# Performance work log

Hardware: AMD Instinct MI355X
Metric: run time of the kernel (lower is better)

The kernel has to match this reference:

```python
import jax, jax.numpy as jnp
import numpy as np


def setup_inputs() -> dict:
    key = jax.random.key(0)
    kq, kk, kv = jax.random.split(key, 3)
    B, L, S, H, E = 2, 2048, 2048, 8, 64
    queries = jax.random.normal(kq, (B, L, H, E), dtype=jnp.float32)
    keys = jax.random.normal(kk, (B, S, H, E), dtype=jnp.float32)
    values = jax.random.normal(kv, (B, S, H, E), dtype=jnp.float32)
    a1 = jnp.float32(1.0)
    a2 = jnp.float32(1.0)
    return {"queries": queries, "keys": keys, "values": values, "a1": a1, "a2": a2}


def reference(queries, keys, values, a1, a2):
    # queries: (B,L,H,E); keys/values: (B,S,H,E)
    E = queries.shape[-1]
    scale = 1.0 / jnp.sqrt(jnp.float32(E))
    # shared QK scores: (B,H,L,S)
    qk = jnp.einsum('blhe,bshe->bhls', queries, keys) * scale
    # sparse branch: relu^2 (dropout = identity in eval)
    ssa = jnp.square(jax.nn.relu(qk))
    ssa_out = jnp.einsum('bhls,bshd->blhd', ssa, values)
    # dense branch: softmax over keys
    dsa = jax.nn.softmax(qk, axis=-1)
    dsa_out = jnp.einsum('bhls,bshd->blhd', dsa, values)
    w1 = jnp.exp(a1)
    w2 = jnp.exp(a2)
    alpha1 = w1 / (w1 + w2)
    alpha2 = w2 / (w1 + w2)
    return alpha1 * ssa_out + alpha2 * dsa_out
```

## Files before the change

### kernel.cpp

```cpp
#include <hip/hip_runtime.h>

typedef short short4v __attribute__((ext_vector_type(4)));
typedef short short8v __attribute__((ext_vector_type(8)));
typedef float float4v __attribute__((ext_vector_type(4)));
typedef unsigned short u16;

#define NB 2
#define NL 2048
#define NS 2048
#define NH 8
#define NE 64
#define HE (NH*NE)
#define NLT (NL/64)
#define NST (NS/64)
#define TILE_U16 4096

static __device__ __forceinline__ unsigned pk2bf(float a, float b) {
  union { float f; unsigned u; } x, y; x.f = a; y.f = b;
  return __builtin_amdgcn_perm(y.u + 0x8000u, x.u + 0x8000u, 0x07060302u);
}

static __device__ __forceinline__ unsigned cvtpk(float a, float b) {
  unsigned r;
  asm("v_cvt_pk_bf16_f32 %0, %1, %2" : "=v"(r) : "v"(a), "v"(b));
  return r;
}

static __device__ __forceinline__ float fexp2(float x) {
  float r;
  asm("v_exp_f32 %0, %1" : "=v"(r) : "v"(x));
  return r;
}

#define GLD16(gp, lp) __builtin_amdgcn_global_load_lds( \
    (const __attribute__((address_space(1))) void*)(gp), \
    (__attribute__((address_space(3))) void*)(lp), 16, 0, 0)

static __device__ __forceinline__ int fK(int s) { return (s & 3) | ((s >> 1) & 4); }

__global__ __launch_bounds__(256)
void prepack(const float* __restrict__ kp, const float* __restrict__ vp,
             u16* __restrict__ kimg, u16* __restrict__ vimg)
{
  __shared__ __align__(16) u16 ldsv[TILE_U16];

  const int bid  = blockIdx.x;
  const int tile = bid >> 1;
  const int doV  = bid & 1;
  const int st = tile & (NST - 1);
  const int bh = tile >> 5;
  const int h  = bh & (NH - 1);
  const int b  = bh >> 3;
  const int s0 = st * 64;
  const size_t base = (size_t)b * NS * HE + h * NE;
  const int tid  = threadIdx.x;
  const int wv   = tid >> 6;
  const int lane = tid & 63;
  const int ln7  = lane & 7;

  if (!doV) {
    u16* kt = kimg + (size_t)tile * TILE_U16;
    for (int slot = tid; slot < 512; slot += 256) {
      const int srow = slot >> 3, p = slot & 7, c = p ^ fK(srow);
      const float* src = kp + base + (size_t)(s0 + srow) * HE + c * 8;
      float4 x0 = *(const float4*)src;
      float4 x1 = *(const float4*)(src + 4);
      unsigned d[4] = { pk2bf(x0.x, x0.y), pk2bf(x0.z, x0.w),
                        pk2bf(x1.x, x1.y), pk2bf(x1.z, x1.w) };
      *(int4*)(kt + slot * 8) = *(const int4*)d;
    }
    return;
  }

  u16* vt = vimg + (size_t)tile * TILE_U16;
  {
    const float* vcol = vp + base + (size_t)(s0 + wv * 16) * HE + lane;
    unsigned vr[8];
    #pragma unroll
    for (int jj = 0; jj < 8; ++jj)
      vr[jj] = pk2bf(vcol[(size_t)(2 * jj) * HE], vcol[(size_t)(2 * jj + 1) * HE]);
    #pragma unroll
    for (int i = 0; i < 2; ++i) {
      const int cs = (2 * wv + i) ^ ln7;
      int4 t4 = make_int4((int)vr[4*i+0], (int)vr[4*i+1],
                          (int)vr[4*i+2], (int)vr[4*i+3]);
      *(int4*)(&ldsv[lane * 64 + cs * 8]) = t4;
    }
  }
  __syncthreads();
  {
    const int4* s = (const int4*)ldsv;
    int4* dst = (int4*)vt;
    dst[tid]       = s[tid];
    dst[tid + 256] = s[tid + 256];
  }
}

__global__ __launch_bounds__(512, 4)
void assa_fwd(const float* __restrict__ qp, const u16* __restrict__ kimg,
              const u16* __restrict__ vimg, const float* __restrict__ a1p,
              const float* __restrict__ a2p, float* __restrict__ op)
{
  __shared__ __align__(16) u16 ldsb[2][2][2 * TILE_U16];

  const int tid  = threadIdx.x;
  const int wv   = tid >> 6;
  const int ws   = wv & 3;
  const int strm = wv >> 2;
  const int lane = tid & 63;
  const int ln15 = lane & 15;
  const int ln7  = lane & 7;
  const int quad = lane >> 4;

  const int bid = blockIdx.x;
  const int bh  = bid & 15;
  const int lt  = bid >> 4;
  const int h   = bh & (NH - 1);
  const int b   = bh >> 3;

  const int lbase = lt * 64 + ws * 16;

  short8v qf0, qf1;
  {
    const float qs = 0.125f * 1.44269504089f;
    const float* qrow = qp + ((size_t)(b * NL + lbase + ln15)) * HE + h * NE + quad * 8;
    float4 q0 = *(const float4*)(qrow);
    float4 q1 = *(const float4*)(qrow + 4);
    float4 q2 = *(const float4*)(qrow + 32);
    float4 q3 = *(const float4*)(qrow + 36);
    unsigned d0[4] = { pk2bf(qs*q0.x, qs*q0.y), pk2bf(qs*q0.z, qs*q0.w),
                       pk2bf(qs*q1.x, qs*q1.y), pk2bf(qs*q1.z, qs*q1.w) };
    unsigned d1[4] = { pk2bf(qs*q2.x, qs*q2.y), pk2bf(qs*q2.z, qs*q2.w),
                       pk2bf(qs*q3.x, qs*q3.y), pk2bf(qs*q3.z, qs*q3.w) };
    qf0 = *(const short8v*)d0;
    qf1 = *(const short8v*)d1;
  }

  short8v ones8;
  #pragma unroll
  for (int j = 0; j < 8; ++j) ones8[j] = (short)0x3F80;

  const size_t tbase = (size_t)bh * NST;

  float4v acc_s[4], acc_d[4], acc_l;
  #pragma unroll
  for (int t = 0; t < 4; ++t)
    #pragma unroll
    for (int r = 0; r < 4; ++r) { acc_s[t][r] = 0.0f; acc_d[t][r] = 0.0f; }
  #pragma unroll
  for (int r = 0; r < 4; ++r) acc_l[r] = 0.0f;

  auto dma_tile = [&](int st, int nb) {
    const int hf = ws & 1;
    const u16* g;
    u16* l;
    if (ws < 2) {
      g = kimg + (tbase + st) * TILE_U16 + hf * 2048 + lane * 8;
      l = &ldsb[strm][nb][hf * 2048];
    } else {
      g = vimg + (tbase + st) * TILE_U16 + hf * 2048 + lane * 8;
      l = &ldsb[strm][nb][TILE_U16 + hf * 2048];
    }
    GLD16(g,        l);
    GLD16(g +  512, l +  512);
    GLD16(g + 1024, l + 1024);
    GLD16(g + 1536, l + 1536);
  };

  dma_tile(strm, 0);

  const int rperm = 8 * (ln15 >> 2) + (ln15 & 3);
  const int fk    = (ln15 & 3) | (((ln15 >> 2) & 1) << 2);

  for (int it = 0; it < NST / 2; ++it) {
    asm volatile("s_waitcnt vmcnt(0)" ::: "memory");
    __builtin_amdgcn_s_barrier();
    asm volatile("" ::: "memory");
    if (it + 1 < NST / 2) dma_tile(2 * (it + 1) + strm, (it + 1) & 1);

    const u16* kb_l = ldsb[strm][it & 1];
    const u16* vb_l = kb_l + TILE_U16;

    #pragma unroll
    for (int U = 0; U < 2; ++U) {
      float4v sa0, sa1;
      #pragma unroll
      for (int r = 0; r < 4; ++r) { sa0[r] = 0.0f; sa1[r] = 0.0f; }
      const u16* krow0 = &kb_l[(32 * U + rperm) * 64];
      const u16* krow1 = krow0 + 4 * 64;
      short8v kf00 = *(const short8v*)(krow0 + (quad ^ fk) * 8);
      short8v kf01 = *(const short8v*)(krow0 + ((4 + quad) ^ fk) * 8);
      short8v kf10 = *(const short8v*)(krow1 + (quad ^ fk) * 8);
      short8v kf11 = *(const short8v*)(krow1 + ((4 + quad) ^ fk) * 8);
      __builtin_amdgcn_s_setprio(1);
      sa0 = __builtin_amdgcn_mfma_f32_16x16x32_bf16(kf00, qf0, sa0, 0, 0, 0);
      sa0 = __builtin_amdgcn_mfma_f32_16x16x32_bf16(kf01, qf1, sa0, 0, 0, 0);
      sa1 = __builtin_amdgcn_mfma_f32_16x16x32_bf16(kf10, qf0, sa1, 0, 0, 0);
      sa1 = __builtin_amdgcn_mfma_f32_16x16x32_bf16(kf11, qf1, sa1, 0, 0, 0);
      __builtin_amdgcn_s_setprio(0);

      float ps[8], pd[8];
      #pragma unroll
      for (int r = 0; r < 4; ++r) {
        float s0 = sa0[r], s1 = sa1[r];
        float r0 = s0 > 0.0f ? s0 : 0.0f;
        float r1 = s1 > 0.0f ? s1 : 0.0f;
        ps[r] = r0 * r0;  ps[4 + r] = r1 * r1;
        pd[r] = fexp2(s0); pd[4 + r] = fexp2(s1);
      }
      unsigned da[4] = { cvtpk(ps[0], ps[1]), cvtpk(ps[2], ps[3]),
                         cvtpk(ps[4], ps[5]), cvtpk(ps[6], ps[7]) };
      unsigned db[4] = { cvtpk(pd[0], pd[1]), cvtpk(pd[2], pd[3]),
                         cvtpk(pd[4], pd[5]), cvtpk(pd[6], pd[7]) };
      short8v as8 = *(const short8v*)da;
      short8v ad8 = *(const short8v*)db;

      __builtin_amdgcn_s_setprio(1);
      acc_l = __builtin_amdgcn_mfma_f32_16x16x32_bf16(ad8, ones8, acc_l, 0, 0, 0);

      #pragma unroll
      for (int t = 0; t < 4; ++t) {
        short8v vf = *(const short8v*)(&vb_l[(t * 16 + ln15) * 64 +
                        (((4 * U + quad) ^ ln7) * 8)]);
        acc_s[t] = __builtin_amdgcn_mfma_f32_16x16x32_bf16(as8, vf, acc_s[t], 0, 0, 0);
        acc_d[t] = __builtin_amdgcn_mfma_f32_16x16x32_bf16(ad8, vf, acc_d[t], 0, 0, 0);
      }
      __builtin_amdgcn_s_setprio(0);
    }
  }

  __syncthreads();
  float* red = (float*)&ldsb[0][0][0];
  const int idx = ws * 64 + lane;
  if (strm == 1) {
    #pragma unroll
    for (int t = 0; t < 4; ++t)
      #pragma unroll
      for (int r = 0; r < 4; ++r) {
        red[(t * 4 + r) * 256 + idx]        = acc_s[t][r];
        red[(16 + t * 4 + r) * 256 + idx]   = acc_d[t][r];
      }
    #pragma unroll
    for (int r = 0; r < 4; ++r)
      red[(32 + r) * 256 + idx] = acc_l[r];
  }
  __syncthreads();
  if (strm == 0) {
    #pragma unroll
    for (int t = 0; t < 4; ++t)
      #pragma unroll
      for (int r = 0; r < 4; ++r) {
        acc_s[t][r] += red[(t * 4 + r) * 256 + idx];
        acc_d[t][r] += red[(16 + t * 4 + r) * 256 + idx];
      }
    #pragma unroll
    for (int r = 0; r < 4; ++r)
      acc_l[r] += red[(32 + r) * 256 + idx];

    const float w1 = __expf(a1p[0]), w2 = __expf(a2p[0]);
    const float al1 = (w1 / (w1 + w2)) * 0.48045301391820142f;
    const float al2 = w2 / (w1 + w2);

    float c_d[4];
    #pragma unroll
    for (int r = 0; r < 4; ++r) c_d[r] = al2 / acc_l[r];

    #pragma unroll
    for (int t = 0; t < 4; ++t) {
      #pragma unroll
      for (int r = 0; r < 4; ++r) {
        float val = al1 * acc_s[t][r] + c_d[r] * acc_d[t][r];
        const int l = lbase + quad * 4 + r;
        const int e = t * 16 + ln15;
        op[((size_t)(b * NL + l)) * HE + h * NE + e] = val;
      }
    }
  }
}

extern "C" void kernel_launch(void* const* d_in, const int* in_sizes, int n_in,
                              void* d_out, int out_size, void* d_ws, size_t ws_size,
                              hipStream_t stream) {
  const float* q  = (const float*)d_in[0];
  const float* k  = (const float*)d_in[1];
  const float* v  = (const float*)d_in[2];
  const float* a1 = (const float*)d_in[3];
  const float* a2 = (const float*)d_in[4];
  float* out = (float*)d_out;
  (void)in_sizes; (void)n_in; (void)out_size; (void)ws_size;

  u16* kimg = (u16*)d_ws;
  u16* vimg = kimg + (size_t)NB * NH * NST * TILE_U16;

  prepack<<<dim3(NB * NH * NST * 2), dim3(256), 0, stream>>>(k, v, kimg, vimg);
  assa_fwd<<<dim3(NB * NH * NLT), dim3(512), 0, stream>>>(q, kimg, vimg, a1, a2, out);
}
```

Measured before the change: 110.3 us.

## Split key tile across waves with two query row-groups per wave, atomic LDS reduction

Each wave now handles 32 query rows (two 16-row groups) against half of a 64-key tile, instead of 16 rows against the full tile. Each K and V fragment loaded from LDS is therefore reused across two query groups, halving LDS fragment traffic per MFMA. The cost is a larger cross-wave reduction: four waves contribute partial sums per row group, merged through LDS atomicAdd after zero-initialising a 36KB region. Register pressure roughly doubles for the accumulators, which may hurt occupancy under the 512x4 launch bound, and the explicit waitcnt+barrier is replaced by __syncthreads.

After: 221.1 us. 2x slower.

```diff
diff --git a/kernel.cpp b/kernel.cpp
--- a/kernel.cpp
+++ b/kernel.cpp
@@ -101,12 +101,15 @@
               const u16* __restrict__ vimg, const float* __restrict__ a1p,
               const float* __restrict__ a2p, float* __restrict__ op)
 {
-  __shared__ __align__(16) u16 ldsb[2][2][2 * TILE_U16];
+  __shared__ __align__(16) unsigned char lds_raw[65536];
+  u16* ldsb = (u16*)lds_raw;
 
   const int tid  = threadIdx.x;
   const int wv   = tid >> 6;
   const int ws   = wv & 3;
   const int strm = wv >> 2;
+  const int sl   = ws >> 1;
+  const int lg   = ws & 1;
   const int lane = tid & 63;
   const int ln15 = lane & 15;
   const int ln7  = lane & 7;
@@ -118,22 +121,33 @@
   const int h   = bh & (NH - 1);
   const int b   = bh >> 3;
 
-  const int lbase = lt * 64 + ws * 16;
-
-  short8v qf0, qf1;
+  const int lbase = lt * 64 + lg * 32;
+
+  short8v qf00, qf01, qf10, qf11;
   {
     const float qs = 0.125f * 1.44269504089f;
-    const float* qrow = qp + ((size_t)(b * NL + lbase + ln15)) * HE + h * NE + quad * 8;
-    float4 q0 = *(const float4*)(qrow);
-    float4 q1 = *(const float4*)(qrow + 4);
-    float4 q2 = *(const float4*)(qrow + 32);
-    float4 q3 = *(const float4*)(qrow + 36);
-    unsigned d0[4] = { pk2bf(qs*q0.x, qs*q0.y), pk2bf(qs*q0.z, qs*q0.w),
-                       pk2bf(qs*q1.x, qs*q1.y), pk2bf(qs*q1.z, qs*q1.w) };
-    unsigned d1[4] = { pk2bf(qs*q2.x, qs*q2.y), pk2bf(qs*q2.z, qs*q2.w),
-                       pk2bf(qs*q3.x, qs*q3.y), pk2bf(qs*q3.z, qs*q3.w) };
-    qf0 = *(const short8v*)d0;
-    qf1 = *(const short8v*)d1;
+    const float* qr0 = qp + ((size_t)(b * NL + lbase + ln15)) * HE + h * NE + quad * 8;
+    float4 a0 = *(const float4*)(qr0);
+    float4 a1 = *(const float4*)(qr0 + 4);
+    float4 a2 = *(const float4*)(qr0 + 32);
+    float4 a3 = *(const float4*)(qr0 + 36);
+    unsigned d0[4] = { pk2bf(qs*a0.x, qs*a0.y), pk2bf(qs*a0.z, qs*a0.w),
+                       pk2bf(qs*a1.x, qs*a1.y), pk2bf(qs*a1.z, qs*a1.w) };
+    unsigned d1[4] = { pk2bf(qs*a2.x, qs*a2.y), pk2bf(qs*a2.z, qs*a2.w),
+                       pk2bf(qs*a3.x, qs*a3.y), pk2bf(qs*a3.z, qs*a3.w) };
+    qf00 = *(const short8v*)d0;
+    qf01 = *(const short8v*)d1;
+    const float* qr1 = qr0 + (size_t)16 * HE;
+    float4 b0 = *(const float4*)(qr1);
+    float4 b1 = *(const float4*)(qr1 + 4);
+    float4 b2 = *(const float4*)(qr1 + 32);
+    float4 b3 = *(const float4*)(qr1 + 36);
+    unsigned e0[4] = { pk2bf(qs*b0.x, qs*b0.y), pk2bf(qs*b0.z, qs*b0.w),
+                       pk2bf(qs*b1.x, qs*b1.y), pk2bf(qs*b1.z, qs*b1.w) };
+    unsigned e1[4] = { pk2bf(qs*b2.x, qs*b2.y), pk2bf(qs*b2.z, qs*b2.w),
+                       pk2bf(qs*b3.x, qs*b3.y), pk2bf(qs*b3.z, qs*b3.w) };
+    qf10 = *(const short8v*)e0;
+    qf11 = *(const short8v*)e1;
   }
 
   short8v ones8;
@@ -142,24 +156,28 @@
 
   const size_t tbase = (size_t)bh * NST;
 
-  float4v acc_s[4], acc_d[4], acc_l;
+  float4v acc_s[2][4], acc_d[2][4], acc_l[2];
   #pragma unroll
-  for (int t = 0; t < 4; ++t)
-    #pragma unroll
-    for (int r = 0; r < 4; ++r) { acc_s[t][r] = 0.0f; acc_d[t][r] = 0.0f; }
-  #pragma unroll
-  for (int r = 0; r < 4; ++r) acc_l[r] = 0.0f;
+  for (int g = 0; g < 2; ++g) {
+    #pragma unroll
+    for (int t = 0; t < 4; ++t)
+      #pragma unroll
+      for (int r = 0; r < 4; ++r) { acc_s[g][t][r] = 0.0f; acc_d[g][t][r] = 0.0f; }
+    #pragma unroll
+    for (int r = 0; r < 4; ++r) acc_l[g][r] = 0.0f;
+  }
 
   auto dma_tile = [&](int st, int nb) {
     const int hf = ws & 1;
+    u16* base = ldsb + (strm * 2 + nb) * (2 * TILE_U16);
     const u16* g;
     u16* l;
     if (ws < 2) {
       g = kimg + (tbase + st) * TILE_U16 + hf * 2048 + lane * 8;
-      l = &ldsb[strm][nb][hf * 2048];
+      l = base + hf * 2048;
     } else {
       g = vimg + (tbase + st) * TILE_U16 + hf * 2048 + lane * 8;
-      l = &ldsb[strm][nb][TILE_U16 + hf * 2048];
+      l = base + TILE_U16 + hf * 2048;
     }
     GLD16(g,        l);
     GLD16(g +  512, l +  512);
@@ -173,36 +191,39 @@
   const int fk    = (ln15 & 3) | (((ln15 >> 2) & 1) << 2);
 
   for (int it = 0; it < NST / 2; ++it) {
-    asm volatile("s_waitcnt vmcnt(0)" ::: "memory");
-    __builtin_amdgcn_s_barrier();
-    asm volatile("" ::: "memory");
+    __syncthreads();
     if (it + 1 < NST / 2) dma_tile(2 * (it + 1) + strm, (it + 1) & 1);
 
-    const u16* kb_l = ldsb[strm][it & 1];
+    const u16* kb_l = ldsb + (strm * 2 + (it & 1)) * (2 * TILE_U16);
     const u16* vb_l = kb_l + TILE_U16;
 
-    #pragma unroll
-    for (int U = 0; U < 2; ++U) {
-      float4v sa0, sa1;
-      #pragma unroll
-      for (int r = 0; r < 4; ++r) { sa0[r] = 0.0f; sa1[r] = 0.0f; }
-      const u16* krow0 = &kb_l[(32 * U + rperm) * 64];
-      const u16* krow1 = krow0 + 4 * 64;
-      short8v kf00 = *(const short8v*)(krow0 + (quad ^ fk) * 8);
-      short8v kf01 = *(const short8v*)(krow0 + ((4 + quad) ^ fk) * 8);
-      short8v kf10 = *(const short8v*)(krow1 + (quad ^ fk) * 8);
-      short8v kf11 = *(const short8v*)(krow1 + ((4 + quad) ^ fk) * 8);
-      __builtin_amdgcn_s_setprio(1);
-      sa0 = __builtin_amdgcn_mfma_f32_16x16x32_bf16(kf00, qf0, sa0, 0, 0, 0);
-      sa0 = __builtin_amdgcn_mfma_f32_16x16x32_bf16(kf01, qf1, sa0, 0, 0, 0);
-      sa1 = __builtin_amdgcn_mfma_f32_16x16x32_bf16(kf10, qf0, sa1, 0, 0, 0);
-      sa1 = __builtin_amdgcn_mfma_f32_16x16x32_bf16(kf11, qf1, sa1, 0, 0, 0);
-      __builtin_amdgcn_s_setprio(0);
-
+    const u16* krow0 = &kb_l[(32 * sl + rperm) * 64];
+    const u16* krow1 = krow0 + 4 * 64;
+    short8v ka0 = *(const short8v*)(krow0 + (quad ^ fk) * 8);
+    short8v ka1 = *(const short8v*)(krow0 + ((4 + quad) ^ fk) * 8);
+    short8v kb0 = *(const short8v*)(krow1 + (quad ^ fk) * 8);
+    short8v kb1 = *(const short8v*)(krow1 + ((4 + quad) ^ fk) * 8);
+
+    float4v z00, z01, z10, z11;
+    #pragma unroll
+    for (int r = 0; r < 4; ++r) { z00[r] = 0.0f; z01[r] = 0.0f; z10[r] = 0.0f; z11[r] = 0.0f; }
+    __builtin_amdgcn_s_setprio(1);
+    z00 = __builtin_amdgcn_mfma_f32_16x16x32_bf16(ka0, qf00, z00, 0, 0, 0);
+    z00 = __builtin_amdgcn_mfma_f32_16x16x32_bf16(ka1, qf01, z00, 0, 0, 0);
+    z01 = __builtin_amdgcn_mfma_f32_16x16x32_bf16(ka0, qf10, z01, 0, 0, 0);
+    z01 = __builtin_amdgcn_mfma_f32_16x16x32_bf16(ka1, qf11, z01, 0, 0, 0);
+    z10 = __builtin_amdgcn_mfma_f32_16x16x32_bf16(kb0, qf00, z10, 0, 0, 0);
+    z10 = __builtin_amdgcn_mfma_f32_16x16x32_bf16(kb1, qf01, z10, 0, 0, 0);
+    z11 = __builtin_amdgcn_mfma_f32_16x16x32_bf16(kb0, qf10, z11, 0, 0, 0);
+    z11 = __builtin_amdgcn_mfma_f32_16x16x32_bf16(kb1, qf11, z11, 0, 0, 0);
+    __builtin_amdgcn_s_setprio(0);
+
+    short8v as8_0, ad8_0, as8_1, ad8_1;
+    {
       float ps[8], pd[8];
       #pragma unroll
       for (int r = 0; r < 4; ++r) {
-        float s0 = sa0[r], s1 = sa1[r];
+        float s0 = z00[r], s1 = z10[r];
         float r0 = s0 > 0.0f ? s0 : 0.0f;
         float r1 = s1 > 0.0f ? s1 : 0.0f;
         ps[r] = r0 * r0;  ps[4 + r] = r1 * r1;
@@ -212,68 +233,88 @@
                          cvtpk(ps[4], ps[5]), cvtpk(ps[6], ps[7]) };
       unsigned db[4] = { cvtpk(pd[0], pd[1]), cvtpk(pd[2], pd[3]),
                          cvtpk(pd[4], pd[5]), cvtpk(pd[6], pd[7]) };
-      short8v as8 = *(const short8v*)da;
-      short8v ad8 = *(const short8v*)db;
-
-      __builtin_amdgcn_s_setprio(1);
-      acc_l = __builtin_amdgcn_mfma_f32_16x16x32_bf16(ad8, ones8, acc_l, 0, 0, 0);
-
-      #pragma unroll
-      for (int t = 0; t < 4; ++t) {
-        short8v vf = *(const short8v*)(&vb_l[(t * 16 + ln15) * 64 +
-                        (((4 * U + quad) ^ ln7) * 8)]);
-        acc_s[t] = __builtin_amdgcn_mfma_f32_16x16x32_bf16(as8, vf, acc_s[t], 0, 0, 0);
-        acc_d[t] = __builtin_amdgcn_mfma_f32_16x16x32_bf16(ad8, vf, acc_d[t], 0, 0, 0);
+      as8_0 = *(const short8v*)da;
+      ad8_0 = *(const short8v*)db;
+    }
+    {
+      float ps[8], pd[8];
+      #pragma unroll
+      for (int r = 0; r < 4; ++r) {
+        float s0 = z01[r], s1 = z11[r];
+        float r0 = s0 > 0.0f ? s0 : 0.0f;
+        float r1 = s1 > 0.0f ? s1 : 0.0f;
+        ps[r] = r0 * r0;  ps[4 + r] = r1 * r1;
+        pd[r] = fexp2(s0); pd[4 + r] = fexp2(s1);
       }
-      __builtin_amdgcn_s_setprio(0);
-    }
+      unsigned da[4] = { cvtpk(ps[0], ps[1]), cvtpk(ps[2], ps[3]),
+                         cvtpk(ps[4], ps[5]), cvtpk(ps[6], ps[7]) };
+      unsigned db[4] = { cvtpk(pd[0], pd[1]), cvtpk(pd[2], pd[3]),
+                         cvtpk(pd[4], pd[5]), cvtpk(pd[6], pd[7]) };
+      as8_1 = *(const short8v*)da;
+      ad8_1 = *(const short8v*)db;
+    }
+
+    acc_l[0] = __builtin_amdgcn_mfma_f32_16x16x32_bf16(ad8_0, ones8, acc_l[0], 0, 0, 0);
+    acc_l[1] = __builtin_amdgcn_mfma_f32_16x16x32_bf16(ad8_1, ones8, acc_l[1], 0, 0, 0);
+
+    __builtin_amdgcn_s_setprio(1);
+    #pragma unroll
+    for (int t = 0; t < 4; ++t) {
+      short8v vf = *(const short8v*)(&vb_l[(t * 16 + ln15) * 64 +
+                      (((4 * sl + quad) ^ ln7) * 8)]);
+      acc_s[0][t] = __builtin_amdgcn_mfma_f32_16x16x32_bf16(as8_0, vf, acc_s[0][t], 0, 0, 0);
+      acc_d[0][t] = __builtin_amdgcn_mfma_f32_16x16x32_bf16(ad8_0, vf, acc_d[0][t], 0, 0, 0);
+      acc_s[1][t] = __builtin_amdgcn_mfma_f32_16x16x32_bf16(as8_1, vf, acc_s[1][t], 0, 0, 0);
+      acc_d[1][t] = __builtin_amdgcn_mfma_f32_16x16x32_bf16(ad8_1, vf, acc_d[1][t], 0, 0, 0);
+    }
+    __builtin_amdgcn_s_setprio(0);
   }
 
   __syncthreads();
-  float* red = (float*)&ldsb[0][0][0];
-  const int idx = ws * 64 + lane;
-  if (strm == 1) {
-    #pragma unroll
-    for (int t = 0; t < 4; ++t)
-      #pragma unroll
-      for (int r = 0; r < 4; ++r) {
-        red[(t * 4 + r) * 256 + idx]        = acc_s[t][r];
-        red[(16 + t * 4 + r) * 256 + idx]   = acc_d[t][r];
-      }
-    #pragma unroll
-    for (int r = 0; r < 4; ++r)
-      red[(32 + r) * 256 + idx] = acc_l[r];
-  }
+  float* red = (float*)lds_raw;
+  for (int i = tid; i < 144 * 64; i += 512) red[i] = 0.0f;
   __syncthreads();
-  if (strm == 0) {
-    #pragma unroll
-    for (int t = 0; t < 4; ++t)
-      #pragma unroll
-      for (int r = 0; r < 4; ++r) {
-        acc_s[t][r] += red[(t * 4 + r) * 256 + idx];
-        acc_d[t][r] += red[(16 + t * 4 + r) * 256 + idx];
-      }
-    #pragma unroll
-    for (int r = 0; r < 4; ++r)
-      acc_l[r] += red[(32 + r) * 256 + idx];
-
+  {
+    const int rb = lg * 72;
+    #pragma unroll
+    for (int l16 = 0; l16 < 2; ++l16) {
+      #pragma unroll
+      for (int t = 0; t < 4; ++t)
+        #pragma unroll
+        for (int r = 0; r < 4; ++r) {
+          atomicAdd(&red[(rb + l16 * 16 + t * 4 + r) * 64 + lane], acc_s[l16][t][r]);
+          atomicAdd(&red[(rb + 32 + l16 * 16 + t * 4 + r) * 64 + lane], acc_d[l16][t][r]);
+        }
+      #pragma unroll
+      for (int r = 0; r < 4; ++r)
+        atomicAdd(&red[(rb + 64 + l16 * 4 + r) * 64 + lane], acc_l[l16][r]);
+    }
+  }
+  __syncthreads();
+
+  if (wv < 2) {
     const float w1 = __expf(a1p[0]), w2 = __expf(a2p[0]);
     const float al1 = (w1 / (w1 + w2)) * 0.48045301391820142f;
     const float al2 = w2 / (w1 + w2);
-
-    float c_d[4];
-    #pragma unroll
-    for (int r = 0; r < 4; ++r) c_d[r] = al2 / acc_l[r];
-
-    #pragma unroll
-    for (int t = 0; t < 4; ++t) {
-      #pragma unroll
-      for (int r = 0; r < 4; ++r) {
-        float val = al1 * acc_s[t][r] + c_d[r] * acc_d[t][r];
-        const int l = lbase + quad * 4 + r;
-        const int e = t * 16 + ln15;
-        op[((size_t)(b * NL + l)) * HE + h * NE + e] = val;
-      }
+    const int rb = lg * 72;
+
+    #pragma unroll
+    for (int l16 = 0; l16 < 2; ++l16) {
+      float inv[4];
+      #pragma unroll
+      for (int r = 0; r < 4; ++r)
+        inv[r] = al2 / red[(rb + 64 + l16 * 4 + r) * 64 + lane];
+      #pragma unroll
+      for (int t = 0; t < 4; ++t)
+        #pragma unroll
+        for (int r = 0; r < 4; ++r) {
+          const int idx = l16 * 16 + t * 4 + r;
+          float val = al1 * red[(rb + idx) * 64 + lane]
+                    + inv[r] * red[(rb + 32 + idx) * 64 + lane];
+          const int l = lbase + l16 * 16 + quad * 4 + r;
+          const int e = t * 16 + ln15;
+          op[((size_t)(b * NL + l)) * HE + h * NE + e] = val;
+        }
     }
   }
 }
```
